# Performance work log

Measured on AMD Instinct MI355X. Metric: run time of the kernel, lower is better.

The kernel has to match this reference:

```python
import jax, jax.numpy as jnp
import numpy as np

VOCAB = 32000
NUM_STATE = 256
NLABEL = 64
BATCH = 128
MAXLEN = 256
# transition init scale chosen so E[e^2]*S*a^2/3 ~= 1 -> per-step magnitude ~constant
TRANS_A = 0.208


def setup_inputs() -> dict:
    key = jax.random.key(0)
    k1, k2, k3, k4 = jax.random.split(key, 4)
    sentences = jax.random.randint(k1, (BATCH, MAXLEN), 0, VOCAB, dtype=jnp.int64)
    # original init: input.weight ~ U(0.5, 0.5) (constant 0.5). Use U(0.25, 0.75) so the
    # emission stays bounded away from 0 (it is divided by) while not being degenerate.
    emb = jax.random.uniform(k2, (VOCAB, NUM_STATE), minval=0.25, maxval=0.75, dtype=jnp.float32)
    transition = jax.random.uniform(k3, (NUM_STATE, NUM_STATE), minval=-TRANS_A, maxval=TRANS_A, dtype=jnp.float32)
    output = jax.random.uniform(k4, (NUM_STATE, NLABEL), minval=-0.5, maxval=0.5, dtype=jnp.float32)
    return {"sentences": sentences, "emb": emb, "transition": transition, "output": output}


def reference(sentences, emb, transition, output):
    # emission: [maxlen, batch, num_state]
    em = emb[sentences.T]

    def step_fwd(carry, e):  # carry: [B,S]
        nxt = jnp.einsum('ij,bj->bi', transition, carry) * e
        return nxt, nxt

    _, fw_rest = jax.lax.scan(step_fwd, em[0], em[1:])
    forwards = jnp.concatenate([em[:1], fw_rest], axis=0)  # [L,B,S]

    em_rev = em[::-1]

    def step_bwd(carry, e):  # uses transition^T
        nxt = jnp.einsum('ji,bj->bi', transition, carry) * e
        return nxt, nxt

    _, bw_rest = jax.lax.scan(step_bwd, em_rev[0], em_rev[1:])
    backwards = jnp.concatenate([em_rev[:1], bw_rest], axis=0)[::-1]  # time-aligned [L,B,S]

    expected_count = forwards * backwards / em
    score = jnp.einsum('lbs,sn->lbn', expected_count, output)
    return score.transpose(1, 0, 2)  # [batch, maxlen, nlabel]
```

## Files before the change

### kernel.cpp

```cpp
#include <hip/hip_runtime.h>
#include <hip/hip_bf16.h>


typedef _Float16 half8 __attribute__((ext_vector_type(8)));
typedef _Float16 half4 __attribute__((ext_vector_type(4)));
typedef float    f32x4 __attribute__((ext_vector_type(4)));
typedef unsigned long long u64;

#define LL 256
#define BB 128
#define SS 256
#define BT 16
#define RSTR8 67
#define RSTRO 65

static __device__ __forceinline__ f32x4 mfma16f(half8 a, half8 b, f32x4 c) {
  return __builtin_amdgcn_mfma_f32_16x16x32_f16(a, b, c, 0, 0, 0);
}

static __device__ __forceinline__ void lds_barrier() {
  __asm__ __volatile__("s_waitcnt lgkmcnt(0)\n\ts_barrier" ::: "memory");
}

static __device__ __forceinline__ u64 pack4(f32x4 v) {
  union { half4 h; u64 u; } x;
  x.h[0] = (_Float16)v[0];
  x.h[1] = (_Float16)v[1];
  x.h[2] = (_Float16)v[2];
  x.h[3] = (_Float16)v[3];
  return x.u;
}

static __device__ __forceinline__ half8 read_frag_s(const u64* plane, int row,
                                                    int kt, int q, int stride8) {
  const int o = row * stride8 + kt * 8 + q * 2;
  union { u64 u[2]; half8 v; } x;
  x.u[0] = plane[o];
  x.u[1] = plane[o + 1];
  return x.v;
}

__global__ __launch_bounds__(512, 2)
void hmm_chain(const int* __restrict__ sent, const float* __restrict__ emb,
               const float* __restrict__ T, _Float16* __restrict__ fwh,
               _Float16* __restrict__ gh)
{
  __shared__ u64 s_carry[2][BT * RSTR8];
  __shared__ int s_tok[BT * 257];

  const int tid  = threadIdx.x;
  const int lane = tid & 63;
  const int w    = tid >> 6;
  const int m    = lane & 15;
  const int q    = lane >> 4;
  const int rot  = (w & 1) << 2;

  const int  bid = blockIdx.x;
  const bool fwd = (bid < 8);
  const int  bg0 = (fwd ? bid : bid - 8) * BT;
  _Float16* const obuf = fwd ? fwh : gh;

  for (int idx = tid; idx < BT * LL; idx += 512) {
    int bb = idx >> 8, l2 = idx & 255;
    s_tok[bb * 257 + l2] = sent[(bg0 + bb) * LL + l2];
  }
  __syncthreads();

  half8 a_hi[2][8];
#pragma unroll
  for (int t = 0; t < 2; ++t) {
    const int r0 = 32 * w + 16 * t + m;
#pragma unroll
    for (int i = 0; i < 8; ++i) {
      const int kb = 32 * (i ^ rot) + 8 * q;
      float v[8];
      if (fwd) {
        f32x4 f0 = *(const f32x4*)(T + r0 * 256 + kb);
        f32x4 f1 = *(const f32x4*)(T + r0 * 256 + kb + 4);
#pragma unroll
        for (int j = 0; j < 4; ++j) { v[j] = f0[j]; v[4 + j] = f1[j]; }
      } else {
#pragma unroll
        for (int j = 0; j < 8; ++j) v[j] = T[(kb + j) * 256 + r0];
      }
      half8 hi;
#pragma unroll
      for (int j = 0; j < 8; ++j) hi[j] = (_Float16)v[j];
      a_hi[t][i] = hi;
    }
  }

  const int l0 = fwd ? 0 : (LL - 1);
  {
    const int tok0 = s_tok[m * 257 + l0];
    f32x4 one = 1.0f;
    const u64 pone = pack4(one);
#pragma unroll
    for (int t = 0; t < 2; ++t) {
      const int st = 32 * w + 16 * t + 4 * q;
      f32x4 e0 = *(const f32x4*)(emb + (size_t)tok0 * 256 + st);
      u64 pc = pack4(e0);
      u64 po = fwd ? pc : pone;
      *(u64*)(obuf + (size_t)(l0 * BB + bg0 + m) * SS + st) = po;
      s_carry[0][m * RSTR8 + 8 * w + 4 * t + q] = pc;
    }
  }

  auto ldem = [&](int su, int t) -> f32x4 {
    su = su < LL ? su : LL - 1;
    const int ln = fwd ? su : (LL - 1) - su;
    const int tk = s_tok[m * 257 + ln];
    return *(const f32x4*)(emb + (size_t)tk * 256 + 32 * w + 16 * t + 4 * q);
  };

  f32x4 em0a = ldem(1, 0), em0b = ldem(1, 1);
  f32x4 em1a = ldem(2, 0), em1b = ldem(2, 1);
  f32x4 em2a = ldem(3, 0), em2b = ldem(3, 1);
  __syncthreads();

  auto step = [&](int ss, f32x4& ea, f32x4& eb) {
    const int l  = fwd ? ss : (LL - 1) - ss;
    const int rb = (ss - 1) & 1, wb = ss & 1;

    const u64* pr = &s_carry[rb][0];
    half8 b0 = read_frag_s(pr, m, 0 ^ rot, q, RSTR8);
    half8 b1 = read_frag_s(pr, m, 1 ^ rot, q, RSTR8);
    half8 b2 = read_frag_s(pr, m, 2 ^ rot, q, RSTR8);
    half8 b3 = read_frag_s(pr, m, 3 ^ rot, q, RSTR8);

    f32x4 e0 = ea, e1 = eb;
    ea = ldem(ss + 3, 0);
    eb = ldem(ss + 3, 1);

    f32x4 aA0 = 0.0f, aB0 = 0.0f, aA1 = 0.0f, aB1 = 0.0f;
    aA0 = mfma16f(a_hi[0][0], b0, aA0);
    aA1 = mfma16f(a_hi[1][0], b0, aA1);
    b0 = read_frag_s(pr, m, 4 ^ rot, q, RSTR8);
    aB0 = mfma16f(a_hi[0][1], b1, aB0);
    aB1 = mfma16f(a_hi[1][1], b1, aB1);
    b1 = read_frag_s(pr, m, 5 ^ rot, q, RSTR8);
    aA0 = mfma16f(a_hi[0][2], b2, aA0);
    aA1 = mfma16f(a_hi[1][2], b2, aA1);
    b2 = read_frag_s(pr, m, 6 ^ rot, q, RSTR8);
    aB0 = mfma16f(a_hi[0][3], b3, aB0);
    aB1 = mfma16f(a_hi[1][3], b3, aB1);
    b3 = read_frag_s(pr, m, 7 ^ rot, q, RSTR8);
    aA0 = mfma16f(a_hi[0][4], b0, aA0);
    aA1 = mfma16f(a_hi[1][4], b0, aA1);
    aB0 = mfma16f(a_hi[0][5], b1, aB0);
    aB1 = mfma16f(a_hi[1][5], b1, aB1);
    aA0 = mfma16f(a_hi[0][6], b2, aA0);
    aA1 = mfma16f(a_hi[1][6], b2, aA1);
    aB0 = mfma16f(a_hi[0][7], b3, aB0);
    aB1 = mfma16f(a_hi[1][7], b3, aB1);

    f32x4 v0 = aA0 + aB0, v1 = aA1 + aB1;
    f32x4 cn0 = v0 * e0,  cn1 = v1 * e1;

    u64 p0 = pack4(cn0), p1 = pack4(cn1);
    s_carry[wb][m * RSTR8 + 8 * w + q]     = p0;
    s_carry[wb][m * RSTR8 + 8 * w + 4 + q] = p1;
    u64 sv0 = fwd ? p0 : pack4(v0);
    u64 sv1 = fwd ? p1 : pack4(v1);
    lds_barrier();
    const int st0 = 32 * w + 4 * q;
    _Float16* orow = obuf + (size_t)(l * BB + bg0 + m) * SS;
    *(u64*)(orow + st0)      = sv0;
    *(u64*)(orow + st0 + 16) = sv1;
  };

  for (int s = 1; s < LL; s += 3) {
    step(s + 0, em0a, em0b);
    step(s + 1, em1a, em1b);
    step(s + 2, em2a, em2b);
  }
}

__global__ __launch_bounds__(256, 2)
void hmm_score(const _Float16* __restrict__ fwh, const _Float16* __restrict__ gh,
               const float* __restrict__ outm, float* __restrict__ score)
{
  __shared__ u64 p_pl[64 * RSTR8];
  __shared__ u64 o_pl[64 * RSTRO];

  const int tid  = threadIdx.x;
  const int lane = tid & 63;
  const int w    = tid >> 6;
  const int rh   = w >> 1;
  const int np   = w & 1;
  const int m    = lane & 15;
  const int q    = lane >> 4;
  const int R0   = blockIdx.x * 64;

  {
    _Float16* o_h = (_Float16*)o_pl;
    for (int i = tid; i < 4096; i += 256) {
      f32x4 v = *(const f32x4*)(outm + i * 4);
      int k = i >> 4, n0 = (i & 15) * 4;
#pragma unroll
      for (int r = 0; r < 4; ++r)
        o_h[(n0 + r) * (RSTRO * 4) + k] = (_Float16)v[r];
    }
  }

  for (int idx = tid; idx < 64 * 64; idx += 256) {
    int row = idx >> 6, c = idx & 63;
    union { u64 u; half4 h; } a, b, p;
    a.u = *(const u64*)(fwh + (size_t)(R0 + row) * 256 + c * 4);
    b.u = *(const u64*)(gh  + (size_t)(R0 + row) * 256 + c * 4);
    p.h = a.h * b.h;
    p_pl[row * RSTR8 + c] = p.u;
  }
  lds_barrier();

  f32x4 acc[2][2];
#pragma unroll
  for (int j = 0; j < 2; ++j)
#pragma unroll
    for (int jn = 0; jn < 2; ++jn) acc[j][jn] = 0.0f;

#pragma unroll
  for (int kt = 0; kt < 8; ++kt) {
    half8 of[2];
#pragma unroll
    for (int jn = 0; jn < 2; ++jn)
      of[jn] = read_frag_s(o_pl, 16 * (2 * np + jn) + m, kt, q, RSTRO);
#pragma unroll
    for (int j = 0; j < 2; ++j) {
      half8 pf = read_frag_s(p_pl, 32 * rh + 16 * j + m, kt, q, RSTR8);
#pragma unroll
      for (int jn = 0; jn < 2; ++jn)
        acc[j][jn] = mfma16f(pf, of[jn], acc[j][jn]);
    }
  }

#pragma unroll
  for (int j = 0; j < 2; ++j) {
#pragma unroll
    for (int jn = 0; jn < 2; ++jn) {
#pragma unroll
      for (int r = 0; r < 4; ++r) {
        int row = R0 + 32 * rh + 16 * j + 4 * q + r;
        int l = row >> 7, b = row & 127;
        score[(size_t)b * 16384 + l * 64 + 16 * (2 * np + jn) + m] = acc[j][jn][r];
      }
    }
  }
}

extern "C" void kernel_launch(void* const* d_in, const int* in_sizes, int n_in,
                              void* d_out, int out_size, void* d_ws, size_t ws_size,
                              hipStream_t stream) {
  (void)in_sizes; (void)n_in; (void)out_size; (void)ws_size;
  const int*   sent = (const int*)d_in[0];
  const float* emb  = (const float*)d_in[1];
  const float* T    = (const float*)d_in[2];
  const float* outm = (const float*)d_in[3];
  _Float16* fwh = (_Float16*)d_ws;
  _Float16* gh  = fwh + (size_t)LL * BB * SS;

  hmm_chain<<<16, 512, 0, stream>>>(sent, emb, T, fwh, gh);
  hmm_score<<<512, 256, 0, stream>>>(fwh, gh, outm, (float*)d_out);
}
```

Measured before the change: 301.6 us.

## Replace per-step block barrier with per-wave LDS progress flags in chain kernel

Drops the block-wide barrier after each recurrence step. Each wave now publishes its step number in a shared flag array after writing its slice of the carry, and before reading spins until all other waves have reached the previous step. The k-tile order is rotated per wave so each wave starts with its own freshly written slice, and the transition fragments are loaded in the matching order. The aim is to let waves drift apart and cut barrier latency on the serial chain. The cost is polling LDS traffic and reliance on volatile LDS ordering, and the spin loop has a bounded bail-out that could silently race if it ever times out.

```diff
diff --git a/kernel.cpp b/kernel.cpp
--- a/kernel.cpp
+++ b/kernel.cpp
@@ -47,13 +47,14 @@
 {
   __shared__ u64 s_carry[2][BT * RSTR8];
   __shared__ int s_tok[BT * 257];
+  __shared__ int flg[8];
+  volatile int* vflg = flg;
 
   const int tid  = threadIdx.x;
   const int lane = tid & 63;
   const int w    = tid >> 6;
   const int m    = lane & 15;
   const int q    = lane >> 4;
-  const int rot  = (w & 1) << 2;
 
   const int  bid = blockIdx.x;
   const bool fwd = (bid < 8);
@@ -72,7 +73,8 @@
     const int r0 = 32 * w + 16 * t + m;
 #pragma unroll
     for (int i = 0; i < 8; ++i) {
-      const int kb = 32 * (i ^ rot) + 8 * q;
+      const int kt = (w + i) & 7;
+      const int kb = 32 * kt + 8 * q;
       float v[8];
       if (fwd) {
         f32x4 f0 = *(const f32x4*)(T + r0 * 256 + kb);
@@ -116,17 +118,34 @@
   f32x4 em0a = ldem(1, 0), em0b = ldem(1, 1);
   f32x4 em1a = ldem(2, 0), em1b = ldem(2, 1);
   f32x4 em2a = ldem(3, 0), em2b = ldem(3, 1);
+
+  if (lane == 0) vflg[w] = 0;
   __syncthreads();
 
   auto step = [&](int ss, f32x4& ea, f32x4& eb) {
-    const int l  = fwd ? ss : (LL - 1) - ss;
-    const int rb = (ss - 1) & 1, wb = ss & 1;
-
+    const int l   = fwd ? ss : (LL - 1) - ss;
+    const int sm1 = ss - 1;
+    const int rb  = (ss - 1) & 1, wb = ss & 1;
     const u64* pr = &s_carry[rb][0];
-    half8 b0 = read_frag_s(pr, m, 0 ^ rot, q, RSTR8);
-    half8 b1 = read_frag_s(pr, m, 1 ^ rot, q, RSTR8);
-    half8 b2 = read_frag_s(pr, m, 2 ^ rot, q, RSTR8);
-    half8 b3 = read_frag_s(pr, m, 3 ^ rot, q, RSTR8);
+
+    {
+      int ok = 0;
+      for (int spin = 0; spin < (1 << 17); ++spin) {
+        int f1 = vflg[(w + 1) & 7], f2 = vflg[(w + 2) & 7];
+        int f3 = vflg[(w + 3) & 7], f4 = vflg[(w + 4) & 7];
+        int f5 = vflg[(w + 5) & 7], f6 = vflg[(w + 6) & 7];
+        int f7 = vflg[(w + 7) & 7];
+        ok = (f1 >= sm1) & (f2 >= sm1) & (f3 >= sm1) & (f4 >= sm1) &
+             (f5 >= sm1) & (f6 >= sm1) & (f7 >= sm1);
+        if (ok) break;
+        __builtin_amdgcn_s_sleep(1);
+      }
+    }
+
+    half8 b0 = read_frag_s(pr, m, (w + 0) & 7, q, RSTR8);
+    half8 b1 = read_frag_s(pr, m, (w + 1) & 7, q, RSTR8);
+    half8 b2 = read_frag_s(pr, m, (w + 2) & 7, q, RSTR8);
+    half8 b3 = read_frag_s(pr, m, (w + 3) & 7, q, RSTR8);
 
     f32x4 e0 = ea, e1 = eb;
     ea = ldem(ss + 3, 0);
@@ -135,16 +154,16 @@
     f32x4 aA0 = 0.0f, aB0 = 0.0f, aA1 = 0.0f, aB1 = 0.0f;
     aA0 = mfma16f(a_hi[0][0], b0, aA0);
     aA1 = mfma16f(a_hi[1][0], b0, aA1);
-    b0 = read_frag_s(pr, m, 4 ^ rot, q, RSTR8);
+    b0 = read_frag_s(pr, m, (w + 4) & 7, q, RSTR8);
     aB0 = mfma16f(a_hi[0][1], b1, aB0);
     aB1 = mfma16f(a_hi[1][1], b1, aB1);
-    b1 = read_frag_s(pr, m, 5 ^ rot, q, RSTR8);
+    b1 = read_frag_s(pr, m, (w + 5) & 7, q, RSTR8);
     aA0 = mfma16f(a_hi[0][2], b2, aA0);
     aA1 = mfma16f(a_hi[1][2], b2, aA1);
-    b2 = read_frag_s(pr, m, 6 ^ rot, q, RSTR8);
+    b2 = read_frag_s(pr, m, (w + 6) & 7, q, RSTR8);
     aB0 = mfma16f(a_hi[0][3], b3, aB0);
     aB1 = mfma16f(a_hi[1][3], b3, aB1);
-    b3 = read_frag_s(pr, m, 7 ^ rot, q, RSTR8);
+    b3 = read_frag_s(pr, m, (w + 7) & 7, q, RSTR8);
     aA0 = mfma16f(a_hi[0][4], b0, aA0);
     aA1 = mfma16f(a_hi[1][4], b0, aA1);
     aB0 = mfma16f(a_hi[0][5], b1, aB0);
@@ -160,9 +179,11 @@
     u64 p0 = pack4(cn0), p1 = pack4(cn1);
     s_carry[wb][m * RSTR8 + 8 * w + q]     = p0;
     s_carry[wb][m * RSTR8 + 8 * w + 4 + q] = p1;
+    __asm__ __volatile__("s_waitcnt lgkmcnt(0)" ::: "memory");
+    if (lane == 0) vflg[w] = ss;
+
     u64 sv0 = fwd ? p0 : pack4(v0);
     u64 sv1 = fwd ? p1 : pack4(v1);
-    lds_barrier();
     const int st0 = 32 * w + 4 * q;
     _Float16* orow = obuf + (size_t)(l * BB + bg0 + m) * SS;
     *(u64*)(orow + st0)      = sv0;
```

New measurement: 395.2 us. 31.0% more time.
